# Performance work log

Measured on AMD Instinct MI355X. Metric: run time of the kernel, lower is better.

Reference implementation:

```python
import jax, jax.numpy as jnp
import numpy as np

DIM = 512
N_TOK = 256
BATCH = 512
HIDDEN = int(DIM * 0.2)          # 102
KEEPED = int(256 * 0.5 * 0.4)    # 51 aggregated tokens
NUM_KEEP = int(np.ceil(N_TOK * 0.5))  # 128 kept tokens
EPS_NORM = 1e-12
EPS_LN = 1e-5


def _l2norm(v, axis=-1):
    n = jnp.linalg.norm(v, axis=axis, keepdims=True)
    return v / jnp.maximum(n, EPS_NORM)


def setup_inputs() -> dict:
    key = jax.random.key(0)
    ks = jax.random.split(key, 8)
    x = jax.random.normal(ks[0], (BATCH, N_TOK, DIM), dtype=jnp.float32)
    cross_attention = jax.random.normal(ks[1], (BATCH, N_TOK), dtype=jnp.float32)
    # TokenAggregation params: LayerNorm(dim) -> Linear(dim,hidden) -> GELU -> Linear(hidden,keeped)
    ln_g = jnp.ones((DIM,), jnp.float32)
    ln_b = jnp.zeros((DIM,), jnp.float32)
    s1 = 1.0 / np.sqrt(DIM)
    W1 = jax.random.uniform(ks[2], (DIM, HIDDEN), jnp.float32, -s1, s1)
    b1 = jax.random.uniform(ks[3], (HIDDEN,), jnp.float32, -s1, s1)
    s2 = 1.0 / np.sqrt(HIDDEN)
    W2 = jax.random.uniform(ks[4], (HIDDEN, KEEPED), jnp.float32, -s2, s2)
    b2 = jax.random.uniform(ks[5], (KEEPED,), jnp.float32, -s2, s2)
    scale = jnp.ones((1, 1, 1), jnp.float32)
    return {"x": x, "cross_attention": cross_attention, "ln_g": ln_g, "ln_b": ln_b,
            "W1": W1, "b1": b1, "W2": W2, "b2": b2, "scale": scale}


def reference(x, cross_attention, ln_g, ln_b, W1, b1, W2, b2, scale):
    # ---- scoring: cosine similarity of each token with the mean token ----
    glo = _l2norm(jnp.mean(x, axis=1, keepdims=True))          # [B,1,C]
    self_att = jnp.sum(glo * _l2norm(x), axis=-1)              # [B,N]
    score = self_att + cross_attention                         # [B,N]

    # ---- TokenSparse: sort descending, split keep / non-keep ----
    idx = jnp.argsort(-score, axis=1)                          # [B,N]
    score_sort = jnp.take_along_axis(score, idx, axis=1)       # [B,N] descending
    keep_idx = idx[:, :NUM_KEEP]                               # [B,K]
    non_idx = idx[:, NUM_KEEP:]                                # [B,N-K]
    sel = jnp.take_along_axis(x, keep_idx[:, :, None], axis=1)       # [B,K,C]
    non = jnp.take_along_axis(x, non_idx[:, :, None], axis=1)        # [B,N-K,C]
    non_w = jax.nn.softmax(score_sort[:, NUM_KEEP:], axis=1)[:, :, None]
    extra = jnp.sum(non * non_w, axis=1, keepdims=True)        # [B,1,C]

    # ---- TokenAggregation: LN -> MLP -> softmax weights -> bmm ----
    mu = jnp.mean(sel, axis=-1, keepdims=True)
    var = jnp.mean((sel - mu) ** 2, axis=-1, keepdims=True)
    h = (sel - mu) / jnp.sqrt(var + EPS_LN) * ln_g + ln_b
    h = jax.nn.gelu(h @ W1 + b1, approximate=False)            # [B,K,H]
    w = h @ W2 + b2                                            # [B,K,P]
    w = jnp.swapaxes(w, 1, 2) * scale                          # [B,P,K]
    w = jax.nn.softmax(w, axis=2)
    aggr = jnp.einsum('bpk,bkc->bpc', w, sel)                  # [B,P,C]

    return jnp.concatenate([aggr, extra], axis=1)              # [B,P+1,C]
```

## Files before the change

### kernel.cpp

```cpp
#include <hip/hip_runtime.h>

#define BB 512
#define TT 256
#define DD 512
#define HH 102
#define PP 51
#define NKEEP 128

typedef unsigned short u16;
typedef unsigned int u32;
typedef unsigned long long u64;
typedef float f32x4 __attribute__((ext_vector_type(4)));
typedef short s16x8 __attribute__((ext_vector_type(8)));

#define MFMA16(A, B, C) __builtin_amdgcn_mfma_f32_16x16x32_bf16((A), (B), (C), 0, 0, 0)

static __device__ __forceinline__ float bf2f(u16 u) {
  u32 v = ((u32)u) << 16;
  float f;
  __builtin_memcpy(&f, &v, 4);
  return f;
}
static __device__ __forceinline__ u16 f2bf(float f) {
  u32 v;
  __builtin_memcpy(&v, &f, 4);
  u32 r = v + 0x7fffu + ((v >> 16) & 1u);
  return (u16)(r >> 16);
}
static __device__ __forceinline__ u32 cvtpk(float a, float b) {
  u32 r;
  asm("v_cvt_pk_bf16_f32 %0, %1, %2" : "=v"(r) : "v"(a), "v"(b));
  return r;
}
static __device__ __forceinline__ float flo16(u32 u) {
  u32 v = u << 16;
  float f;
  __builtin_memcpy(&f, &v, 4);
  return f;
}
static __device__ __forceinline__ float fhi16(u32 u) {
  u32 v = u & 0xffff0000u;
  float f;
  __builtin_memcpy(&f, &v, 4);
  return f;
}
static __device__ __forceinline__ s16x8 mkfrag4(u32 a, u32 b, u32 c, u32 d) {
  u32 t[4] = {a, b, c, d};
  s16x8 f;
  __builtin_memcpy(&f, t, 16);
  return f;
}
static __device__ __forceinline__ s16x8 mkfrag2(u64 a, u64 b) {
  u64 t[2] = {a, b};
  s16x8 f;
  __builtin_memcpy(&f, t, 16);
  return f;
}
static __device__ __forceinline__ u64 trread(u32 addr, int imm) {
  u64 d;
  asm volatile("ds_read_b64_tr_b16 %0, %1 offset:%2" : "=v"(d) : "v"(addr), "i"(imm));
  return d;
}

__global__ __launch_bounds__(1024, 4) void k_score(
    const float* __restrict__ x, const float* __restrict__ ca,
    const float* __restrict__ w1, const float* __restrict__ w2,
    float* __restrict__ out, int* __restrict__ keepg,
    float* __restrict__ muk, float* __restrict__ ivk,
    u16* __restrict__ w1th, u16* __restrict__ w1tl,
    u16* __restrict__ w2th, u16* __restrict__ w2tl) {
  const int tid = threadIdx.x;

  if (blockIdx.x >= BB) {
    const int e0 = (blockIdx.x - BB) * 4096;
#pragma unroll
    for (int i = 0; i < 4; ++i) {
      const int e = e0 + i * 1024 + tid;
      if (e < 57344) {
        const int p = e >> 9, k = e & 511;
        const float v = (p < HH) ? w1[(size_t)k * HH + p] : 0.f;
        const u16 hi = f2bf(v);
        w1th[e] = hi;
        w1tl[e] = f2bf(v - bf2f(hi));
      } else {
        const int e2 = e - 57344;
        const int p = e2 >> 7, j = e2 & 127;
        const float v = (p < PP && j < HH) ? w2[(size_t)j * PP + p] : 0.f;
        const u16 hi = f2bf(v);
        w2th[e2] = hi;
        w2tl[e2] = f2bf(v - bf2f(hi));
      }
    }
    return;
  }

  __shared__ float part[8 * 512];
  __shared__ float glo[DD];
  __shared__ float sc[TT];
  __shared__ float ss[TT];
  __shared__ int perm[TT];
  __shared__ float wq[NKEEP];
  __shared__ float red[128];
  __shared__ float mls[TT], ils[TT];
  int* pc = (int*)part;

  const int b = blockIdx.x;
  const float* xb = x + (size_t)b * TT * DD;

  {
    int c4 = (tid & 127) * 4, tg = tid >> 7;
    float4 a = {0.f, 0.f, 0.f, 0.f};
    const float* p0 = xb + tg * 32 * DD + c4;
    for (int t = 0; t < 32; ++t) {
      float4 v = *(const float4*)(p0 + t * DD);
      a.x += v.x; a.y += v.y; a.z += v.z; a.w += v.w;
    }
    *(float4*)&part[tg * 512 + c4] = a;
  }
  __syncthreads();
  if (tid < 128) {
    int c4 = tid * 4;
    float4 m = {0.f, 0.f, 0.f, 0.f};
    for (int g = 0; g < 8; ++g) {
      float4 v = *(const float4*)&part[g * 512 + c4];
      m.x += v.x; m.y += v.y; m.z += v.z; m.w += v.w;
    }
    m.x *= (1.f / TT); m.y *= (1.f / TT); m.z *= (1.f / TT); m.w *= (1.f / TT);
    *(float4*)&glo[c4] = m;
    red[tid] = m.x * m.x + m.y * m.y + m.z * m.z + m.w * m.w;
  }
  __syncthreads();
  for (int s = 64; s > 0; s >>= 1) {
    if (tid < s) red[tid] += red[tid + s];
    __syncthreads();
  }
  if (tid < 128) {
    float inv = 1.f / fmaxf(sqrtf(red[0]), 1e-12f);
    int c4 = tid * 4;
    float4 m = *(float4*)&glo[c4];
    m.x *= inv; m.y *= inv; m.z *= inv; m.w *= inv;
    *(float4*)&glo[c4] = m;
  }
  __syncthreads();

  {
    const int w = tid >> 6, lane = tid & 63;
    float gl[8];
#pragma unroll
    for (int j = 0; j < 8; ++j) gl[j] = glo[lane * 8 + j];
    for (int i = 0; i < 16; ++i) {
      int t = w * 16 + i;
      const float* xr = xb + t * DD + lane * 8;
      float4 r0 = *(const float4*)xr;
      float4 r1 = *(const float4*)(xr + 4);
      float vs[8] = {r0.x, r0.y, r0.z, r0.w, r1.x, r1.y, r1.z, r1.w};
      float s1 = 0.f, s2 = 0.f, dt = 0.f;
#pragma unroll
      for (int j = 0; j < 8; ++j) {
        s1 += vs[j];
        s2 += vs[j] * vs[j];
        dt += vs[j] * gl[j];
      }
      for (int m = 32; m; m >>= 1) {
        s1 += __shfl_xor(s1, m);
        s2 += __shfl_xor(s2, m);
        dt += __shfl_xor(dt, m);
      }
      if (lane == 0) {
        sc[t] = dt / fmaxf(sqrtf(s2), 1e-12f) + ca[b * TT + t];
        float mu = s1 * (1.f / DD);
        float var = s2 * (1.f / DD) - mu * mu;
        mls[t] = mu;
        ils[t] = rsqrtf(var + 1e-5f);
      }
    }
  }
  __syncthreads();

  {
    int t = tid & 255, ch = tid >> 8;
    float st = sc[t];
    int cnt = 0;
    for (int j = ch * 64; j < ch * 64 + 64; ++j) {
      float sj = sc[j];
      cnt += (sj > st) || (sj == st && j < t);
    }
    pc[ch * 256 + t] = cnt;
  }
  __syncthreads();
  if (tid < 256) {
    int rank = pc[tid] + pc[256 + tid] + pc[512 + tid] + pc[768 + tid];
    perm[rank] = tid;
    ss[rank] = sc[tid];
  }
  __syncthreads();

  if (tid < 128) {
    float e = expf(ss[NKEEP + tid] - ss[NKEEP]);
    wq[tid] = e;
    red[tid] = e;
  }
  __syncthreads();
  for (int s = 64; s > 0; s >>= 1) {
    if (tid < s) red[tid] += red[tid + s];
    __syncthreads();
  }
  if (tid < 128) {
    wq[tid] *= (1.f / red[0]);
    const int pm = perm[tid];
    keepg[b * NKEEP + tid] = pm;
    muk[b * NKEEP + tid] = mls[pm];
    ivk[b * NKEEP + tid] = ils[pm];
  }
  __syncthreads();

  {
    int c4 = (tid & 127) * 4, tg = tid >> 7;
    float4 a = {0.f, 0.f, 0.f, 0.f};
    for (int q = tg * 16; q < tg * 16 + 16; ++q) {
      int tok = perm[NKEEP + q] & 255;
      float w = wq[q];
      float4 v = *(const float4*)(xb + tok * DD + c4);
      a.x += w * v.x; a.y += w * v.y; a.z += w * v.z; a.w += w * v.w;
    }
    *(float4*)&part[tg * 512 + c4] = a;
  }
  __syncthreads();
  if (tid < 128) {
    int c4 = tid * 4;
    float4 m = {0.f, 0.f, 0.f, 0.f};
    for (int g = 0; g < 8; ++g) {
      float4 v = *(const float4*)&part[g * 512 + c4];
      m.x += v.x; m.y += v.y; m.z += v.z; m.w += v.w;
    }
    *(float4*)(out + ((size_t)b * 52 + 51) * DD + c4) = m;
  }
}

__global__ __launch_bounds__(512, 4) void k_fused(
    const float* __restrict__ x,
    const u16* __restrict__ w1th, const u16* __restrict__ w1tl,
    const u16* __restrict__ w2th, const u16* __restrict__ w2tl,
    const float* __restrict__ lng, const float* __restrict__ lnb,
    const float* __restrict__ b1, const float* __restrict__ b2,
    const float* __restrict__ scale, const int* __restrict__ keepg,
    const float* __restrict__ mukg, const float* __restrict__ ivkg,
    float* __restrict__ out) {
  __shared__ __align__(16) char SEL[32768];
  __shared__ __align__(16) float wt[64 * 132];
  __shared__ __align__(16) float lnGs[DD], lnBs[DD];
  __shared__ float mus[NKEEP], ivs[NKEEP];
  __shared__ int keeps[NKEEP];
  __shared__ float b1s[112], b2s[64];
  __shared__ float sscale;

  const int b = blockIdx.x;
  const int tid = threadIdx.x;
  const int w = tid >> 6;
  const int lane = tid & 63;
  const int cl = lane & 15;
  const int g2 = lane >> 4;

  if (tid < NKEEP) {
    keeps[tid] = keepg[b * NKEEP + tid] & 255;
    mus[tid] = mukg[b * NKEEP + tid];
    ivs[tid] = ivkg[b * NKEEP + tid];
  }
  for (int i = tid; i < DD; i += 512) {
    lnGs[i] = lng[i];
    lnBs[i] = lnb[i];
  }
  if (tid < 112) b1s[tid] = (tid < HH) ? b1[tid] : 0.f;
  if (tid < 64) b2s[tid] = (tid < PP) ? b2[tid] : 0.f;
  if (tid == 0) sscale = scale[0];
  __syncthreads();

  const float* xb = x + (size_t)b * TT * DD;

  const int rowm = 16 * w + cl;
  const int tok = keeps[rowm];
  const float mu = mus[rowm], iv = ivs[rowm];
  const float nmuiv = -mu * iv;
  const float* xrow = xb + (size_t)tok * DD;

  f32x4 acc1[7];
#pragma unroll
  for (int n = 0; n < 7; ++n) acc1[n] = (f32x4){0.f, 0.f, 0.f, 0.f};

#pragma unroll 4
  for (int kk = 0; kk < 16; ++kk) {
    const int d0 = kk * 32 + g2 * 8;
    float4 xv0 = *(const float4*)(xrow + d0);
    float4 xv1 = *(const float4*)(xrow + d0 + 4);
    float4 gg0 = *(const float4*)&lnGs[d0];
    float4 gg1 = *(const float4*)&lnGs[d0 + 4];
    float4 bb0 = *(const float4*)&lnBs[d0];
    float4 bb1 = *(const float4*)&lnBs[d0 + 4];
    float y0 = fmaf(fmaf(xv0.x, iv, nmuiv), gg0.x, bb0.x);
    float y1 = fmaf(fmaf(xv0.y, iv, nmuiv), gg0.y, bb0.y);
    float y2 = fmaf(fmaf(xv0.z, iv, nmuiv), gg0.z, bb0.z);
    float y3 = fmaf(fmaf(xv0.w, iv, nmuiv), gg0.w, bb0.w);
    float y4 = fmaf(fmaf(xv1.x, iv, nmuiv), gg1.x, bb1.x);
    float y5 = fmaf(fmaf(xv1.y, iv, nmuiv), gg1.y, bb1.y);
    float y6 = fmaf(fmaf(xv1.z, iv, nmuiv), gg1.z, bb1.z);
    float y7 = fmaf(fmaf(xv1.w, iv, nmuiv), gg1.w, bb1.w);
    u32 h01 = cvtpk(y0, y1), h23 = cvtpk(y2, y3);
    u32 h45 = cvtpk(y4, y5), h67 = cvtpk(y6, y7);
    u32 l01 = cvtpk(y0 - flo16(h01), y1 - fhi16(h01));
    u32 l23 = cvtpk(y2 - flo16(h23), y3 - fhi16(h23));
    u32 l45 = cvtpk(y4 - flo16(h45), y5 - fhi16(h45));
    u32 l67 = cvtpk(y6 - flo16(h67), y7 - fhi16(h67));
    const s16x8 fh = mkfrag4(h01, h23, h45, h67);
    const s16x8 fl = mkfrag4(l01, l23, l45, l67);
    const int bcol = cl * 512 + d0;
#pragma unroll
    for (int n = 0; n < 7; ++n) {
      const s16x8 bh = *(const s16x8*)(w1th + n * 8192 + bcol);
      const s16x8 bl = *(const s16x8*)(w1tl + n * 8192 + bcol);
      acc1[n] = MFMA16(fh, bh, acc1[n]);
      acc1[n] = MFMA16(fl, bh, acc1[n]);
      acc1[n] = MFMA16(fh, bl, acc1[n]);
    }
  }

#pragma unroll
  for (int n = 0; n < 7; ++n) {
    const int col = 16 * n + cl;
    const float bia = b1s[col];
#pragma unroll
    for (int r = 0; r < 4; ++r) {
      const int row = 16 * w + 4 * g2 + r;
      float v = acc1[n][r] + bia;
      float ge = 0.5f * v * (1.f + erff(v * 0.70710678118f));
      const int byteoff = (row * 256 + col * 2) ^ ((row & 7) << 4);
      *(u16*)(SEL + byteoff) = f2bf(ge);
    }
  }
  for (int i = tid; i < 1024; i += 512) {
    const int row = i >> 3;
    const int col = 112 + 2 * (i & 7);
    const int byteoff = (row * 256 + col * 2) ^ ((row & 7) << 4);
    *(u32*)(SEL + byteoff) = 0u;
  }
  __syncthreads();

  f32x4 acc2[4];
#pragma unroll
  for (int n = 0; n < 4; ++n) acc2[n] = (f32x4){0.f, 0.f, 0.f, 0.f};
  {
    const int row2 = 16 * w + cl;
#pragma unroll
    for (int kk = 0; kk < 4; ++kk) {
      const int byteoff = (row2 * 256 + kk * 64 + g2 * 16) ^ ((row2 & 7) << 4);
      const s16x8 ha = *(const s16x8*)(SEL + byteoff);
      const int bcol2 = cl * 128 + kk * 32 + g2 * 8;
#pragma unroll
      for (int n = 0; n < 4; ++n) {
        const s16x8 bh = *(const s16x8*)(w2th + n * 2048 + bcol2);
        const s16x8 bl = *(const s16x8*)(w2tl + n * 2048 + bcol2);
        acc2[n] = MFMA16(ha, bh, acc2[n]);
        acc2[n] = MFMA16(ha, bl, acc2[n]);
      }
    }
  }
  {
    const float scv = sscale;
#pragma unroll
    for (int n = 0; n < 4; ++n) {
      const int p = 16 * n + cl;
#pragma unroll
      for (int r = 0; r < 4; ++r) {
        const int k = 16 * w + 4 * g2 + r;
        wt[p * 132 + k] = (acc2[n][r] + b2s[p]) * scv;
      }
    }
  }
  __syncthreads();

  for (int p = w; p < PP; p += 8) {
    float v0 = wt[p * 132 + lane], v1 = wt[p * 132 + 64 + lane];
    float mx = fmaxf(v0, v1);
    for (int m = 32; m; m >>= 1) mx = fmaxf(mx, __shfl_xor(mx, m));
    float e0 = expf(v0 - mx), e1 = expf(v1 - mx);
    float s = e0 + e1;
    for (int m = 32; m; m >>= 1) s += __shfl_xor(s, m);
    float is = 1.f / s;
    wt[p * 132 + lane] = e0 * is;
    wt[p * 132 + 64 + lane] = e1 * is;
  }
  __syncthreads();

  const int mb = w >> 2;
  const int nsub = w & 3;
  s16x8 ah0[4], al0[4], ah1[4], al1[4];
  {
    const int pr0 = 32 * mb + cl;
    const int pr1 = pr0 + 16;
#pragma unroll
    for (int kk = 0; kk < 4; ++kk) {
      f32x4 wa = *(const f32x4*)&wt[pr0 * 132 + kk * 32 + 8 * g2];
      f32x4 wb = *(const f32x4*)&wt[pr0 * 132 + kk * 32 + 8 * g2 + 4];
      u32 a0 = cvtpk(wa.x, wa.y), a1 = cvtpk(wa.z, wa.w);
      u32 a2 = cvtpk(wb.x, wb.y), a3 = cvtpk(wb.z, wb.w);
      ah0[kk] = mkfrag4(a0, a1, a2, a3);
      al0[kk] = mkfrag4(cvtpk(wa.x - flo16(a0), wa.y - fhi16(a0)),
                        cvtpk(wa.z - flo16(a1), wa.w - fhi16(a1)),
                        cvtpk(wb.x - flo16(a2), wb.y - fhi16(a2)),
                        cvtpk(wb.z - flo16(a3), wb.w - fhi16(a3)));
      f32x4 wc = *(const f32x4*)&wt[pr1 * 132 + kk * 32 + 8 * g2];
      f32x4 wd = *(const f32x4*)&wt[pr1 * 132 + kk * 32 + 8 * g2 + 4];
      u32 c0 = cvtpk(wc.x, wc.y), c1 = cvtpk(wc.z, wc.w);
      u32 c2 = cvtpk(wd.x, wd.y), c3 = cvtpk(wd.z, wd.w);
      ah1[kk] = mkfrag4(c0, c1, c2, c3);
      al1[kk] = mkfrag4(cvtpk(wc.x - flo16(c0), wc.y - fhi16(c0)),
                        cvtpk(wc.z - flo16(c1), wc.w - fhi16(c1)),
                        cvtpk(wd.x - flo16(c2), wd.y - fhi16(c2)),
                        cvtpk(wd.z - flo16(c3), wd.w - fhi16(c3)));
    }
  }
  const u32 trbase = (u32)(size_t)SEL + nsub * 1024 + g2 * 128 + 8 * cl;

  for (int ch = 0; ch < 8; ++ch) {
    const int cbase = ch * 64;
#pragma unroll
    for (int s = 0; s < 4; ++s) {
      const int u = tid + s * 512;
      const int k = u >> 4, c4g = u & 15;
      const float4 v = *(const float4*)(xb + (size_t)keeps[k] * DD + cbase + 4 * c4g);
      u32 h01 = cvtpk(v.x, v.y), h23 = cvtpk(v.z, v.w);
      u32 q01 = cvtpk(v.x - flo16(h01), v.y - fhi16(h01));
      u32 q23 = cvtpk(v.z - flo16(h23), v.w - fhi16(h23));
      const int kl = k & 31;
      const int boff = ((k >> 5) * 8 + (c4g >> 2) * 2 + ((kl >> 2) & 1)) * 512 +
                       (kl >> 3) * 128 + (kl & 3) * 32 + (c4g & 3) * 8;
      *(u64*)(SEL + boff) = ((u64)h23 << 32) | h01;
      *(u64*)(SEL + 16384 + boff) = ((u64)q23 << 32) | q01;
    }
    __syncthreads();

    f32x4 acg0 = (f32x4){0.f, 0.f, 0.f, 0.f};
    f32x4 acg1 = (f32x4){0.f, 0.f, 0.f, 0.f};
    u64 th[4][2], tl[4][2];
#pragma unroll
    for (int kk = 0; kk < 4; ++kk) {
      th[kk][0] = trread(trbase, kk * 4096);
      th[kk][1] = trread(trbase, kk * 4096 + 512);
      tl[kk][0] = trread(trbase, kk * 4096 + 16384);
      tl[kk][1] = trread(trbase, kk * 4096 + 16896);
    }
    asm volatile("s_waitcnt lgkmcnt(0)" ::: "memory");
    __builtin_amdgcn_sched_barrier(0);
#pragma unroll
    for (int kk = 0; kk < 4; ++kk) {
      const s16x8 bh = mkfrag2(th[kk][0], th[kk][1]);
      const s16x8 bl = mkfrag2(tl[kk][0], tl[kk][1]);
      acg0 = MFMA16(ah0[kk], bh, acg0);
      acg0 = MFMA16(al0[kk], bh, acg0);
      acg0 = MFMA16(ah0[kk], bl, acg0);
      acg1 = MFMA16(ah1[kk], bh, acg1);
      acg1 = MFMA16(al1[kk], bh, acg1);
      acg1 = MFMA16(ah1[kk], bl, acg1);
    }
    const int ccol = cbase + 16 * nsub + cl;
#pragma unroll
    for (int r = 0; r < 4; ++r) {
      const int p0 = 32 * mb + 4 * g2 + r;
      if (p0 < PP) out[((size_t)b * 52 + p0) * DD + ccol] = acg0[r];
      const int p1 = 32 * mb + 16 + 4 * g2 + r;
      if (p1 < PP) out[((size_t)b * 52 + p1) * DD + ccol] = acg1[r];
    }
    __syncthreads();
  }
}

extern "C" void kernel_launch(void* const* d_in, const int* in_sizes, int n_in,
                              void* d_out, int out_size, void* d_ws, size_t ws_size,
                              hipStream_t stream) {
  const float* x = (const float*)d_in[0];
  const float* ca = (const float*)d_in[1];
  const float* lng = (const float*)d_in[2];
  const float* lnb = (const float*)d_in[3];
  const float* w1 = (const float*)d_in[4];
  const float* b1 = (const float*)d_in[5];
  const float* w2 = (const float*)d_in[6];
  const float* b2 = (const float*)d_in[7];
  const float* scale = (const float*)d_in[8];
  float* out = (float*)d_out;

  char* ws = (char*)d_ws;
  int* keepg = (int*)ws;
  float* muk = (float*)(ws + 262144);
  float* ivk = (float*)(ws + 524288);
  u16* w1th = (u16*)(ws + 786432);
  u16* w1tl = (u16*)(ws + 901120);
  u16* w2th = (u16*)(ws + 1015808);
  u16* w2tl = (u16*)(ws + 1032192);

  k_score<<<BB + 16, 1024, 0, stream>>>(x, ca, w1, w2, out, keepg, muk, ivk,
                                        w1th, w1tl, w2th, w2tl);
  k_fused<<<BB, 512, 0, stream>>>(x, w1th, w1tl, w2th, w2tl, lng, lnb, b1, b2,
                                  scale, keepg, muk, ivk, out);
}
```

Measured before the change: 606.5 us.

## Stage W1/W2 weights into LDS via async global_load_lds with double-buffered prefetch

The first MLP GEMM now streams bf16 hi/lo W1 tiles into a double-buffered, XOR-swizzled LDS pool with global_load_lds, prefetching the next tile and the next x slice while MFMAs run on the current one. W2 is also staged into LDS, and the aggregation loop prefetches the next chunk of gathered x rows into registers before computing the current one. This replaces repeated per-wave global reads of the weight matrices with shared LDS reads and overlaps global latency with compute. In exchange the kernel uses about 66KB of LDS, occupancy hints change (k_fused drops to 2 blocks per CU, k_score raised to 8), and extra barriers are added.

```diff
diff --git a/kernel.cpp b/kernel.cpp
--- a/kernel.cpp
+++ b/kernel.cpp
@@ -15,6 +15,11 @@
 
 #define MFMA16(A, B, C) __builtin_amdgcn_mfma_f32_16x16x32_bf16((A), (B), (C), 0, 0, 0)
 
+#define GLOAD16(gsrc, ldst)                                                     \
+  __builtin_amdgcn_global_load_lds(                                             \
+      (const __attribute__((address_space(1))) u32*)(gsrc),                     \
+      (__attribute__((address_space(3))) u32*)(ldst), 16, 0, 0)
+
 static __device__ __forceinline__ float bf2f(u16 u) {
   u32 v = ((u32)u) << 16;
   float f;
@@ -62,7 +67,7 @@
   return d;
 }
 
-__global__ __launch_bounds__(1024, 4) void k_score(
+__global__ __launch_bounds__(1024, 8) void k_score(
     const float* __restrict__ x, const float* __restrict__ ca,
     const float* __restrict__ w1, const float* __restrict__ w2,
     float* __restrict__ out, int* __restrict__ keepg,
@@ -237,7 +242,7 @@
   }
 }
 
-__global__ __launch_bounds__(512, 4) void k_fused(
+__global__ __launch_bounds__(512, 2) void k_fused(
     const float* __restrict__ x,
     const u16* __restrict__ w1th, const u16* __restrict__ w1tl,
     const u16* __restrict__ w2th, const u16* __restrict__ w2tl,
@@ -246,8 +251,7 @@
     const float* __restrict__ scale, const int* __restrict__ keepg,
     const float* __restrict__ mukg, const float* __restrict__ ivkg,
     float* __restrict__ out) {
-  __shared__ __align__(16) char SEL[32768];
-  __shared__ __align__(16) float wt[64 * 132];
+  __shared__ __align__(16) char pool[66560];
   __shared__ __align__(16) float lnGs[DD], lnBs[DD];
   __shared__ float mus[NKEEP], ivs[NKEEP];
   __shared__ int keeps[NKEEP];
@@ -283,46 +287,101 @@
   const float nmuiv = -mu * iv;
   const float* xrow = xb + (size_t)tok * DD;
 
+  const int swz7 = cl & 7;
+  const int bA0 = cl * 128 + ((g2 ^ swz7) << 4);
+  const int bA1 = cl * 128 + (((4 + g2) ^ swz7) << 4);
+
   f32x4 acc1[7];
 #pragma unroll
   for (int n = 0; n < 7; ++n) acc1[n] = (f32x4){0.f, 0.f, 0.f, 0.f};
 
-#pragma unroll 4
-  for (int kk = 0; kk < 16; ++kk) {
-    const int d0 = kk * 32 + g2 * 8;
-    float4 xv0 = *(const float4*)(xrow + d0);
-    float4 xv1 = *(const float4*)(xrow + d0 + 4);
-    float4 gg0 = *(const float4*)&lnGs[d0];
-    float4 gg1 = *(const float4*)&lnGs[d0 + 4];
-    float4 bb0 = *(const float4*)&lnBs[d0];
-    float4 bb1 = *(const float4*)&lnBs[d0 + 4];
-    float y0 = fmaf(fmaf(xv0.x, iv, nmuiv), gg0.x, bb0.x);
-    float y1 = fmaf(fmaf(xv0.y, iv, nmuiv), gg0.y, bb0.y);
-    float y2 = fmaf(fmaf(xv0.z, iv, nmuiv), gg0.z, bb0.z);
-    float y3 = fmaf(fmaf(xv0.w, iv, nmuiv), gg0.w, bb0.w);
-    float y4 = fmaf(fmaf(xv1.x, iv, nmuiv), gg1.x, bb1.x);
-    float y5 = fmaf(fmaf(xv1.y, iv, nmuiv), gg1.y, bb1.y);
-    float y6 = fmaf(fmaf(xv1.z, iv, nmuiv), gg1.z, bb1.z);
-    float y7 = fmaf(fmaf(xv1.w, iv, nmuiv), gg1.w, bb1.w);
-    u32 h01 = cvtpk(y0, y1), h23 = cvtpk(y2, y3);
-    u32 h45 = cvtpk(y4, y5), h67 = cvtpk(y6, y7);
-    u32 l01 = cvtpk(y0 - flo16(h01), y1 - fhi16(h01));
-    u32 l23 = cvtpk(y2 - flo16(h23), y3 - fhi16(h23));
-    u32 l45 = cvtpk(y4 - flo16(h45), y5 - fhi16(h45));
-    u32 l67 = cvtpk(y6 - flo16(h67), y7 - fhi16(h67));
-    const s16x8 fh = mkfrag4(h01, h23, h45, h67);
-    const s16x8 fl = mkfrag4(l01, l23, l45, l67);
-    const int bcol = cl * 512 + d0;
-#pragma unroll
-    for (int n = 0; n < 7; ++n) {
-      const s16x8 bh = *(const s16x8*)(w1th + n * 8192 + bcol);
-      const s16x8 bl = *(const s16x8*)(w1tl + n * 8192 + bcol);
-      acc1[n] = MFMA16(fh, bh, acc1[n]);
-      acc1[n] = MFMA16(fl, bh, acc1[n]);
-      acc1[n] = MFMA16(fh, bl, acc1[n]);
-    }
-  }
-
+#define STAGE_W1(tt, dst)                                                      \
+  {                                                                            \
+    _Pragma("unroll") for (int i_ = 0; i_ < 4; ++i_) {                         \
+      const int j_ = w + 8 * i_;                                               \
+      if (j_ < 28) {                                                           \
+        const int s_ = j_ * 64 + lane;                                         \
+        const int part_ = (j_ >= 14);                                          \
+        const int sr_ = s_ - part_ * 896;                                      \
+        const int row_ = sr_ >> 3, uu_ = sr_ & 7;                              \
+        const u16* src_ = (part_ ? w1tl : w1th) + row_ * 512 + (tt)*64 +       \
+                          ((uu_ ^ (row_ & 7)) << 3);                           \
+        GLOAD16(src_, (dst) + j_ * 1024);                                      \
+      }                                                                        \
+    }                                                                          \
+  }
+
+  float4 xc0 = *(const float4*)(xrow + g2 * 8);
+  float4 xc1 = *(const float4*)(xrow + g2 * 8 + 4);
+  float4 xc2 = *(const float4*)(xrow + 32 + g2 * 8);
+  float4 xc3 = *(const float4*)(xrow + 32 + g2 * 8 + 4);
+  STAGE_W1(0, pool);
+  __syncthreads();
+
+#pragma unroll 1
+  for (int t = 0; t < 8; ++t) {
+    float4 xn0, xn1, xn2, xn3;
+    if (t < 7) {
+      STAGE_W1(t + 1, pool + ((t + 1) & 1) * 28672);
+      const float* xr2 = xrow + (t + 1) * 64 + g2 * 8;
+      xn0 = *(const float4*)xr2;
+      xn1 = *(const float4*)(xr2 + 4);
+      xn2 = *(const float4*)(xr2 + 32);
+      xn3 = *(const float4*)(xr2 + 36);
+    }
+    const char* wbr = pool + (t & 1) * 28672;
+#pragma unroll
+    for (int kh = 0; kh < 2; ++kh) {
+      const int d0 = t * 64 + kh * 32 + g2 * 8;
+      const float4 xv0 = kh ? xc2 : xc0;
+      const float4 xv1 = kh ? xc3 : xc1;
+      const float4 gg0 = *(const float4*)&lnGs[d0];
+      const float4 gg1 = *(const float4*)&lnGs[d0 + 4];
+      const float4 bb0 = *(const float4*)&lnBs[d0];
+      const float4 bb1 = *(const float4*)&lnBs[d0 + 4];
+      float y0 = fmaf(fmaf(xv0.x, iv, nmuiv), gg0.x, bb0.x);
+      float y1 = fmaf(fmaf(xv0.y, iv, nmuiv), gg0.y, bb0.y);
+      float y2 = fmaf(fmaf(xv0.z, iv, nmuiv), gg0.z, bb0.z);
+      float y3 = fmaf(fmaf(xv0.w, iv, nmuiv), gg0.w, bb0.w);
+      float y4 = fmaf(fmaf(xv1.x, iv, nmuiv), gg1.x, bb1.x);
+      float y5 = fmaf(fmaf(xv1.y, iv, nmuiv), gg1.y, bb1.y);
+      float y6 = fmaf(fmaf(xv1.z, iv, nmuiv), gg1.z, bb1.z);
+      float y7 = fmaf(fmaf(xv1.w, iv, nmuiv), gg1.w, bb1.w);
+      u32 h01 = cvtpk(y0, y1), h23 = cvtpk(y2, y3);
+      u32 h45 = cvtpk(y4, y5), h67 = cvtpk(y6, y7);
+      u32 l01 = cvtpk(y0 - flo16(h01), y1 - fhi16(h01));
+      u32 l23 = cvtpk(y2 - flo16(h23), y3 - fhi16(h23));
+      u32 l45 = cvtpk(y4 - flo16(h45), y5 - fhi16(h45));
+      u32 l67 = cvtpk(y6 - flo16(h67), y7 - fhi16(h67));
+      const s16x8 fh = mkfrag4(h01, h23, h45, h67);
+      const s16x8 fl = mkfrag4(l01, l23, l45, l67);
+      const int bA = kh ? bA1 : bA0;
+#pragma unroll
+      for (int n = 0; n < 7; ++n) {
+        const s16x8 bh = *(const s16x8*)(wbr + n * 2048 + bA);
+        const s16x8 bl = *(const s16x8*)(wbr + 14336 + n * 2048 + bA);
+        acc1[n] = MFMA16(fh, bh, acc1[n]);
+        acc1[n] = MFMA16(fl, bh, acc1[n]);
+        acc1[n] = MFMA16(fh, bl, acc1[n]);
+      }
+    }
+    __syncthreads();
+    if (t < 7) { xc0 = xn0; xc1 = xn1; xc2 = xn2; xc3 = xn3; }
+  }
+
+  char* W2b = pool + 32768;
+  {
+#pragma unroll
+    for (int i = 0; i < 4; ++i) {
+      const int j2 = w + 8 * i;
+      const int part = (j2 >= 16);
+      const int jj = j2 - part * 16;
+      const int s = jj * 64 + lane;
+      const int row = s >> 4, uu = s & 15;
+      const u16* src = (part ? w2tl : w2th) + row * 128 + ((uu ^ (row & 15)) << 3);
+      GLOAD16(src, W2b + part * 16384 + jj * 1024);
+    }
+  }
 #pragma unroll
   for (int n = 0; n < 7; ++n) {
     const int col = 16 * n + cl;
@@ -333,14 +392,14 @@
       float v = acc1[n][r] + bia;
       float ge = 0.5f * v * (1.f + erff(v * 0.70710678118f));
       const int byteoff = (row * 256 + col * 2) ^ ((row & 7) << 4);
-      *(u16*)(SEL + byteoff) = f2bf(ge);
+      *(u16*)(pool + byteoff) = f2bf(ge);
     }
   }
   for (int i = tid; i < 1024; i += 512) {
     const int row = i >> 3;
     const int col = 112 + 2 * (i & 7);
     const int byteoff = (row * 256 + col * 2) ^ ((row & 7) << 4);
-    *(u32*)(SEL + byteoff) = 0u;
+    *(u32*)(pool + byteoff) = 0u;
   }
   __syncthreads();
 
@@ -352,17 +411,19 @@
 #pragma unroll
     for (int kk = 0; kk < 4; ++kk) {
       const int byteoff = (row2 * 256 + kk * 64 + g2 * 16) ^ ((row2 & 7) << 4);
-      const s16x8 ha = *(const s16x8*)(SEL + byteoff);
-      const int bcol2 = cl * 128 + kk * 32 + g2 * 8;
+      const s16x8 ha = *(const s16x8*)(pool + byteoff);
+      const int bB = cl * 256 + (((kk * 4 + g2) ^ cl) << 4);
 #pragma unroll
       for (int n = 0; n < 4; ++n) {
-        const s16x8 bh = *(const s16x8*)(w2th + n * 2048 + bcol2);
-        const s16x8 bl = *(const s16x8*)(w2tl + n * 2048 + bcol2);
+        const s16x8 bh = *(const s16x8*)(W2b + n * 4096 + bB);
+        const s16x8 bl = *(const s16x8*)(W2b + 16384 + n * 4096 + bB);
         acc2[n] = MFMA16(ha, bh, acc2[n]);
         acc2[n] = MFMA16(ha, bl, acc2[n]);
       }
     }
   }
+  __syncthreads();
+  float* wt = (float*)(pool + 32768);
   {
     const float scv = sscale;
 #pragma unroll
@@ -392,6 +453,20 @@
 
   const int mb = w >> 2;
   const int nsub = w & 3;
+
+  const int c4g = tid & 15;
+  const int k0 = tid >> 4;
+  const float* xcb = xb + 4 * c4g;
+  const int tk0 = keeps[k0], tk1 = keeps[k0 + 32];
+  const int tk2 = keeps[k0 + 64], tk3 = keeps[k0 + 96];
+  const int base_b = (((c4g >> 2) * 2 + ((k0 >> 2) & 1)) << 9) +
+                     ((k0 >> 3) << 7) + ((k0 & 3) << 5) + ((c4g & 3) << 3);
+
+  float4 pv0 = *(const float4*)(xcb + (size_t)tk0 * DD);
+  float4 pv1 = *(const float4*)(xcb + (size_t)tk1 * DD);
+  float4 pv2 = *(const float4*)(xcb + (size_t)tk2 * DD);
+  float4 pv3 = *(const float4*)(xcb + (size_t)tk3 * DD);
+
   s16x8 ah0[4], al0[4], ah1[4], al1[4];
   {
     const int pr0 = 32 * mb + cl;
@@ -418,26 +493,32 @@
                         cvtpk(wd.z - flo16(c3), wd.w - fhi16(c3)));
     }
   }
-  const u32 trbase = (u32)(size_t)SEL + nsub * 1024 + g2 * 128 + 8 * cl;
-
+  const u32 trbase = (u32)(size_t)pool + nsub * 1024 + g2 * 128 + 8 * cl;
+
+#define SELW(v, bo)                                                            \
+  {                                                                            \
+    u32 h01_ = cvtpk((v).x, (v).y), h23_ = cvtpk((v).z, (v).w);                \
+    u32 q01_ = cvtpk((v).x - flo16(h01_), (v).y - fhi16(h01_));                \
+    u32 q23_ = cvtpk((v).z - flo16(h23_), (v).w - fhi16(h23_));                \
+    *(u64*)(pool + (bo)) = ((u64)h23_ << 32) | h01_;                           \
+    *(u64*)(pool + 16384 + (bo)) = ((u64)q23_ << 32) | q01_;                   \
+  }
+
+#pragma unroll 1
   for (int ch = 0; ch < 8; ++ch) {
-    const int cbase = ch * 64;
-#pragma unroll
-    for (int s = 0; s < 4; ++s) {
-      const int u = tid + s * 512;
-      const int k = u >> 4, c4g = u & 15;
-      const float4 v = *(const float4*)(xb + (size_t)keeps[k] * DD + cbase + 4 * c4g);
-      u32 h01 = cvtpk(v.x, v.y), h23 = cvtpk(v.z, v.w);
-      u32 q01 = cvtpk(v.x - flo16(h01), v.y - fhi16(h01));
-      u32 q23 = cvtpk(v.z - flo16(h23), v.w - fhi16(h23));
-      const int kl = k & 31;
-      const int boff = ((k >> 5) * 8 + (c4g >> 2) * 2 + ((kl >> 2) & 1)) * 512 +
-                       (kl >> 3) * 128 + (kl & 3) * 32 + (c4g & 3) * 8;
-      *(u64*)(SEL + boff) = ((u64)h23 << 32) | h01;
-      *(u64*)(SEL + 16384 + boff) = ((u64)q23 << 32) | q01;
-    }
+    SELW(pv0, base_b);
+    SELW(pv1, base_b + 4096);
+    SELW(pv2, base_b + 8192);
+    SELW(pv3, base_b + 12288);
     __syncthreads();
-
+    float4 nv0, nv1, nv2, nv3;
+    if (ch < 7) {
+      const float* xnp = xcb + (ch + 1) * 64;
+      nv0 = *(const float4*)(xnp + (size_t)tk0 * DD);
+      nv1 = *(const float4*)(xnp + (size_t)tk1 * DD);
+      nv2 = *(const float4*)(xnp + (size_t)tk2 * DD);
+      nv3 = *(const float4*)(xnp + (size_t)tk3 * DD);
+    }
     f32x4 acg0 = (f32x4){0.f, 0.f, 0.f, 0.f};
     f32x4 acg1 = (f32x4){0.f, 0.f, 0.f, 0.f};
     u64 th[4][2], tl[4][2];
@@ -461,7 +542,7 @@
       acg1 = MFMA16(al1[kk], bh, acg1);
       acg1 = MFMA16(ah1[kk], bl, acg1);
     }
-    const int ccol = cbase + 16 * nsub + cl;
+    const int ccol = ch * 64 + 16 * nsub + cl;
 #pragma unroll
     for (int r = 0; r < 4; ++r) {
       const int p0 = 32 * mb + 4 * g2 + r;
@@ -470,6 +551,7 @@
       if (p1 < PP) out[((size_t)b * 52 + p1) * DD + ccol] = acg1[r];
     }
     __syncthreads();
+    if (ch < 7) { pv0 = nv0; pv1 = nv1; pv2 = nv2; pv3 = nv3; }
   }
 }
 
```

New measurement: 523.2 us. -13.7%, faster.
